# Optimization experiments

Measured on AMD Instinct MI355X. Metric: run time of the kernel, lower is better.

Reference implementation:

```python
import jax, jax.numpy as jnp
import numpy as np

N = 30000      # num_nodes
E = 480000     # num_edges
NF = 128       # node_features
EF = 64        # edge_features
HID = 256      # hidden_dim
L = 4          # num_layers
H = 8          # heads
D = HID // H   # per-head dim = 32
SCALE = 0.02


def _ln(x, g, b, eps=1e-5):
    m = x.mean(-1, keepdims=True)
    v = ((x - m) ** 2).mean(-1, keepdims=True)
    return (x - m) * jax.lax.rsqrt(v + eps) * g + b


def _mlp_head(x, W1, b1, W2, b2):
    return jax.nn.sigmoid(jax.nn.relu(x @ W1 + b1) @ W2 + b2)


def setup_inputs() -> dict:
    key = jax.random.key(0)
    ks = jax.random.split(key, 32)
    r = lambda k, shp: SCALE * jax.random.normal(k, shp, dtype=jnp.float32)
    inp = {
        'x': jax.random.normal(ks[0], (N, NF), dtype=jnp.float32),
        'edge_attr': jax.random.normal(ks[1], (E, EF), dtype=jnp.float32),
        'edge_index': jax.random.randint(ks[2], (2, E), 0, N, dtype=jnp.int32),
        # encoders
        'enc_Wn': r(ks[3], (NF, HID)), 'enc_bn': jnp.zeros((HID,), jnp.float32),
        'enc_We': r(ks[4], (EF, HID)), 'enc_be': jnp.zeros((HID,), jnp.float32),
        # stacked TransformerConv params for L layers
        'Wq': r(ks[5], (L, HID, HID)), 'bq': jnp.zeros((L, HID), jnp.float32),
        'Wk': r(ks[6], (L, HID, HID)), 'bk': jnp.zeros((L, HID), jnp.float32),
        'Wv': r(ks[7], (L, HID, HID)), 'bv': jnp.zeros((L, HID), jnp.float32),
        'We': r(ks[8], (L, HID, HID)),  # lin_edge has no bias in PyG
        'Wsk': r(ks[9], (L, HID, HID)), 'bsk': jnp.zeros((L, HID), jnp.float32),
        # shared LayerNorm (module reuses self.norm every layer)
        'ln_g': jnp.ones((HID,), jnp.float32), 'ln_b': jnp.zeros((HID,), jnp.float32),
        # contagion predictor
        'cp_W1': r(ks[10], (HID, HID // 2)), 'cp_b1': jnp.zeros((HID // 2,), jnp.float32),
        'cp_W2': r(ks[11], (HID // 2, 1)), 'cp_b2': jnp.zeros((1,), jnp.float32),
        # systemic risk predictor
        'sp_W1': r(ks[12], (HID, HID // 2)), 'sp_b1': jnp.zeros((HID // 2,), jnp.float32),
        'sp_W2': r(ks[13], (HID // 2, 1)), 'sp_b2': jnp.zeros((1,), jnp.float32),
    }
    return inp


def reference(x, edge_attr, edge_index, enc_Wn, enc_bn, enc_We, enc_be,
              Wq, bq, Wk, bk, Wv, bv, We, Wsk, bsk, ln_g, ln_b,
              cp_W1, cp_b1, cp_W2, cp_b2, sp_W1, sp_b1, sp_W2, sp_b2):
    src, dst = edge_index[0], edge_index[1]
    h = x @ enc_Wn + enc_bn                 # [N,HID]
    e = edge_attr @ enc_We + enc_be         # [E,HID]
    inv_sqrt_d = 1.0 / jnp.sqrt(jnp.asarray(D, h.dtype))
    for l in range(L):
        # TransformerConv: query at dst, key/value at src, edge bias on both k and v
        q = (h @ Wq[l] + bq[l]).reshape(N, H, D)[dst]            # [E,H,D]
        ke = (e @ We[l]).reshape(E, H, D)                        # [E,H,D]
        k = (h @ Wk[l] + bk[l]).reshape(N, H, D)[src] + ke
        v = (h @ Wv[l] + bv[l]).reshape(N, H, D)[src] + ke
        score = (q * k).sum(-1) * inv_sqrt_d                     # [E,H]
        smax = jax.ops.segment_max(score, dst, num_segments=N)   # [N,H]
        p = jnp.exp(score - smax[dst])
        denom = jax.ops.segment_sum(p, dst, num_segments=N)
        alpha = p / (denom[dst] + 1e-16)                         # scatter-softmax
        agg = jax.ops.segment_sum(alpha[..., None] * v, dst, num_segments=N)
        out = agg.reshape(N, HID) + h @ Wsk[l] + bsk[l]          # concat heads + root skip
        h = _ln(h + out, ln_g, ln_b)                             # residual + shared LN (eval: no dropout)
    g = h.mean(0, keepdims=True)                                 # [1,HID] global mean pool
    contagion_risk = _mlp_head(h, cp_W1, cp_b1, cp_W2, cp_b2)    # [N,1]
    systemic_risk = _mlp_head(g, sp_W1, sp_b1, sp_W2, sp_b2)     # [1,1]
    return h, g, contagion_risk, systemic_risk
```

## Files before the change

kernel.cpp:

```cpp
#include <hip/hip_runtime.h>
#include <cstddef>
#include <cstdint>

#define NN 30000
#define EE 480000
#define NFD 128
#define EFD 64
#define HID 256
#define NL 4
#define NH 8

#define DT_BF16 0
#define DT_F32  1
#define DT_EXT  2

#define OFF_WT  ((size_t)65787648)
#define MIN_B   ((size_t)68015872)
#define MIN_A   ((size_t)129455872)

#define WT_ENC 0
#define WT_LAYER(l) (32768 + (size_t)(l) * 262144)
#define WT_CP1 (32768 + (size_t)1048576)

typedef short bf16x8 __attribute__((ext_vector_type(8)));
typedef unsigned short us8 __attribute__((ext_vector_type(8)));
typedef float f32x4 __attribute__((ext_vector_type(4)));

__device__ __forceinline__ float bf2f(unsigned short u) {
  union { unsigned int i; float f; } v; v.i = ((unsigned int)u) << 16; return v.f;
}
__device__ __forceinline__ unsigned short f2bf(float f) {
  union { float f; unsigned int i; } v; v.f = f;
  unsigned int i = v.i;
  return (unsigned short)((i + 0x7FFFu + ((i >> 16) & 1u)) >> 16);
}
struct F4 { float x, y, z, w; };
__device__ __forceinline__ F4 load4bf(const unsigned short* p) {
  ushort4 u = *reinterpret_cast<const ushort4*>(p);
  F4 f; f.x = bf2f(u.x); f.y = bf2f(u.y); f.z = bf2f(u.z); f.w = bf2f(u.w);
  return f;
}
__device__ __forceinline__ F4 load4f(const float* p) {
  float4 t = *reinterpret_cast<const float4*>(p);
  F4 f; f.x = t.x; f.y = t.y; f.z = t.z; f.w = t.w; return f;
}
__device__ __forceinline__ F4 load4any(const void* p, size_t idx, int f32) {
  return f32 ? load4f((const float*)p + idx) : load4bf((const unsigned short*)p + idx);
}
__device__ __forceinline__ float load1any(const void* p, size_t idx, int f32) {
  return f32 ? ((const float*)p)[idx] : bf2f(((const unsigned short*)p)[idx]);
}
__device__ __forceinline__ void store1any(void* p, size_t idx, float v, int f32) {
  if (f32) ((float*)p)[idx] = v; else ((unsigned short*)p)[idx] = f2bf(v);
}

__global__ void probe_dtype(const void* __restrict__ ln_g, int* __restrict__ flag) {
  unsigned int u = *(const unsigned int*)ln_g;
  *flag = ((u & 0xFFFFu) == 0u) ? 1 : 0;
}

__global__ void wt_build(const void* __restrict__ enc_Wn,
                         const void* __restrict__ Wq, const void* __restrict__ Wk,
                         const void* __restrict__ Wv, const void* __restrict__ Wsk,
                         const void* __restrict__ cp_W1,
                         unsigned short* __restrict__ Wt, const int* __restrict__ flagp)
{
  const int f = *flagp;
  size_t idx = (size_t)blockIdx.x * 256 + threadIdx.x;
  if (idx < 32768) {
    int n = idx >> 7, k = idx & 127;
    Wt[WT_ENC + idx] = f2bf(load1any(enc_Wn, (size_t)k * 256 + n, f));
  } else if (idx < 32768 + 1048576) {
    size_t off = idx - 32768;
    int l = off >> 18;
    int which = (off >> 16) & 3;
    size_t e = off & 65535;
    int n = e >> 8, k = e & 255;
    const void* W = (which == 0) ? Wq : (which == 1) ? Wk : (which == 2) ? Wv : Wsk;
    Wt[idx] = f2bf(load1any(W, (size_t)l * 65536 + (size_t)k * 256 + n, f));
  } else if (idx < 32768 + 1048576 + 32768) {
    size_t e = idx - 32768 - 1048576;
    int n = e >> 8, k = e & 255;
    Wt[idx] = f2bf(load1any(cp_W1, (size_t)k * 128 + n, f));
  }
}

template<bool OUT_F32, bool RELU>
__global__ __launch_bounds__(256) void mfma_gemm(
    const void* __restrict__ Av, int aMode,
    const unsigned short* __restrict__ Bt,
    const void* __restrict__ biasv, size_t biasEl, int biasMode,
    void* __restrict__ Cv, int ldC, int cOff,
    int M, int K, const int* __restrict__ flagp)
{
  const int f = *flagp;
  const int aF32 = (aMode == DT_EXT) ? f : aMode;
  const int biF32 = (biasMode == DT_EXT) ? f : biasMode;

  __shared__ unsigned short Al[128][40];
  __shared__ unsigned short Bl[64][40];
  const int bm = blockIdx.x * 128;
  const int bn = blockIdx.y * 64;
  const int tid = threadIdx.x;
  const int wv = tid >> 6, lane = tid & 63;
  const int l16 = lane & 15, quad = lane >> 4;

  f32x4 acc[2][4];
#pragma unroll
  for (int i = 0; i < 2; i++)
#pragma unroll
    for (int j = 0; j < 4; j++) acc[i][j] = (f32x4){0.f, 0.f, 0.f, 0.f};

  const int ar = tid >> 1;
  const int ah = (tid & 1) << 4;
  const int bnr = tid >> 2;
  const int bk8 = (tid & 3) << 3;

  for (int k0 = 0; k0 < K; k0 += 32) {
    us8 w0, w1;
    int gr = bm + ar;
    if (gr < M) {
      if (!aF32) {
        const unsigned short* ap = (const unsigned short*)Av + (size_t)gr * K + k0 + ah;
        w0 = *(const us8*)ap;
        w1 = *(const us8*)(ap + 8);
      } else {
        const float* ap = (const float*)Av + (size_t)gr * K + k0 + ah;
        float4 u0 = *(const float4*)ap;
        float4 u1 = *(const float4*)(ap + 4);
        float4 u2 = *(const float4*)(ap + 8);
        float4 u3 = *(const float4*)(ap + 12);
        w0[0] = f2bf(u0.x); w0[1] = f2bf(u0.y); w0[2] = f2bf(u0.z); w0[3] = f2bf(u0.w);
        w0[4] = f2bf(u1.x); w0[5] = f2bf(u1.y); w0[6] = f2bf(u1.z); w0[7] = f2bf(u1.w);
        w1[0] = f2bf(u2.x); w1[1] = f2bf(u2.y); w1[2] = f2bf(u2.z); w1[3] = f2bf(u2.w);
        w1[4] = f2bf(u3.x); w1[5] = f2bf(u3.y); w1[6] = f2bf(u3.z); w1[7] = f2bf(u3.w);
      }
    } else {
      w0 = (us8)0; w1 = (us8)0;
    }
    *(us8*)&Al[ar][ah] = w0;
    *(us8*)&Al[ar][ah + 8] = w1;
    *(us8*)&Bl[bnr][bk8] = *(const us8*)&Bt[(size_t)(bn + bnr) * K + k0 + bk8];
    __syncthreads();

    bf16x8 a0 = *(const bf16x8*)&Al[wv * 32 + l16][quad * 8];
    bf16x8 a1 = *(const bf16x8*)&Al[wv * 32 + 16 + l16][quad * 8];
#pragma unroll
    for (int tn = 0; tn < 4; tn++) {
      bf16x8 b = *(const bf16x8*)&Bl[tn * 16 + l16][quad * 8];
      acc[0][tn] = __builtin_amdgcn_mfma_f32_16x16x32_bf16(a0, b, acc[0][tn], 0, 0, 0);
      acc[1][tn] = __builtin_amdgcn_mfma_f32_16x16x32_bf16(a1, b, acc[1][tn], 0, 0, 0);
    }
    __syncthreads();
  }

#pragma unroll
  for (int tm = 0; tm < 2; tm++) {
#pragma unroll
    for (int tn = 0; tn < 4; tn++) {
      int col = bn + tn * 16 + l16;
      float bias = load1any(biasv, biasEl + col, biF32);
#pragma unroll
      for (int r = 0; r < 4; r++) {
        int row = bm + wv * 32 + tm * 16 + quad * 4 + r;
        if (row < M) {
          float v = acc[tm][tn][r] + bias;
          if (RELU) v = fmaxf(v, 0.f);
          size_t off = (size_t)row * ldC + cOff + col;
          if (OUT_F32) ((float*)Cv)[off] = v;
          else ((unsigned short*)Cv)[off] = f2bf(v);
        }
      }
    }
  }
}

__global__ void fold_kernel(const void* __restrict__ enc_We,
                            const void* __restrict__ enc_be,
                            const void* __restrict__ We_all,
                            float* __restrict__ Mfold, const int* __restrict__ flagp)
{
  const int f = *flagp;
  int idx = blockIdx.x * blockDim.x + threadIdx.x;
  if (idx >= NL * 65 * HID) return;
  int l = idx / (65 * HID);
  int rc = idx - l * 65 * HID;
  int row = rc >> 8;
  int col = rc & 255;
  size_t Wbase = (size_t)l * HID * HID;
  float acc = 0.f;
  if (row < 64) {
    for (int k = 0; k < HID; k++)
      acc += load1any(enc_We, (size_t)row * HID + k, f) * load1any(We_all, Wbase + (size_t)k * HID + col, f);
  } else {
    for (int k = 0; k < HID; k++)
      acc += load1any(enc_be, k, f) * load1any(We_all, Wbase + (size_t)k * HID + col, f);
  }
  Mfold[idx] = acc;
}

__global__ void hist_kernel(const int* __restrict__ dst, int* __restrict__ rp) {
  int e = blockIdx.x * 256 + threadIdx.x;
  if (e < EE) atomicAdd(&rp[dst[e]], 1);
}

__global__ __launch_bounds__(1024) void scan_kernel(int* __restrict__ rp) {
  __shared__ int part[1024];
  int t = threadIdx.x;
  int base = t * 30;
  int loc[30];
  int sum = 0;
#pragma unroll
  for (int i = 0; i < 30; i++) {
    int idx = base + i;
    int v = (idx < NN) ? rp[idx] : 0;
    loc[i] = v; sum += v;
  }
  part[t] = sum;
  __syncthreads();
  for (int off = 1; off < 1024; off <<= 1) {
    int v = (t >= off) ? part[t - off] : 0;
    __syncthreads();
    part[t] += v;
    __syncthreads();
  }
  int run = (t == 0) ? 0 : part[t - 1];
#pragma unroll
  for (int i = 0; i < 30; i++) {
    int idx = base + i;
    if (idx < NN) { rp[idx] = run; run += loc[i]; }
    else if (idx == NN) { rp[NN] = run; }
  }
}

__global__ void scatter_kernel(const int* __restrict__ src, const int* __restrict__ dst,
                               const int* __restrict__ rp, int* __restrict__ cnt2,
                               int2* __restrict__ sed) {
  int e = blockIdx.x * 256 + threadIdx.x;
  if (e >= EE) return;
  int d = dst[e];
  int pos = rp[d] + atomicAdd(&cnt2[d], 1);
  int2 v; v.x = src[e]; v.y = e;
  sed[pos] = v;
}

__global__ void ea_build(const int2* __restrict__ sed, const void* __restrict__ edge_attr,
                         unsigned short* __restrict__ ea_srt, const int* __restrict__ flagp) {
  const int f = *flagp;
  int gid = blockIdx.x * 256 + threadIdx.x;
  int pos = gid >> 4;
  int sub = (gid & 15) * 4;
  int e = sed[pos].y;
  F4 v = load4any(edge_attr, (size_t)e * EFD + sub, f);
  ushort4 o; o.x = f2bf(v.x); o.y = f2bf(v.y); o.z = f2bf(v.z); o.w = f2bf(v.w);
  *reinterpret_cast<ushort4*>(ea_srt + (size_t)pos * EFD + sub) = o;
}

template<bool SORTED>
__global__ __launch_bounds__(256) void edge_fused(
    const int* __restrict__ rp, const int2* __restrict__ sed,
    const unsigned short* __restrict__ Qb, const unsigned short* __restrict__ KV,
    const unsigned short* __restrict__ ea_srt,
    const void* __restrict__ edge_attr,
    const float* __restrict__ Mf,
    const unsigned short* __restrict__ Sb,
    unsigned short* __restrict__ hb,
    const void* __restrict__ ln_g, const void* __restrict__ ln_b,
    const int* __restrict__ flagp)
{
  __shared__ float wl[4][8][68];
  const int f = *flagp;
  const int wv = threadIdx.x >> 6;
  const int nw = blockIdx.x * 4 + wv;
  const int lane = threadIdx.x & 63;
  const int hd = lane >> 3;
  const int j = lane & 7;
  const int c4 = lane * 4;

  const size_t rowb = (size_t)nw * HID;
  F4 q4 = load4bf(Qb + rowb + c4);

  float q32[32];
#pragma unroll
  for (int i = 0; i < 8; i++) {
    F4 t = load4bf(Qb + rowb + hd * 32 + i * 4);
    q32[i * 4 + 0] = t.x; q32[i * 4 + 1] = t.y; q32[i * 4 + 2] = t.z; q32[i * 4 + 3] = t.w;
  }
  float t8[8];
#pragma unroll
  for (int kk = 0; kk < 8; kk++) {
    const float* Mrow = Mf + (size_t)(j * 8 + kk) * HID + hd * 32;
    float a = 0.f;
#pragma unroll
    for (int cc = 0; cc < 8; cc++) {
      float4 m4 = *reinterpret_cast<const float4*>(Mrow + cc * 4);
      a = fmaf(m4.x, q32[cc * 4 + 0], a);
      a = fmaf(m4.y, q32[cc * 4 + 1], a);
      a = fmaf(m4.z, q32[cc * 4 + 2], a);
      a = fmaf(m4.w, q32[cc * 4 + 3], a);
    }
    t8[kk] = a;
  }
  F4 b4 = load4f(Mf + (size_t)64 * HID + c4);
  float s0 = q4.x * b4.x + q4.y * b4.y + q4.z * b4.z + q4.w * b4.w;
  s0 += __shfl_xor(s0, 1);
  s0 += __shfl_xor(s0, 2);
  s0 += __shfl_xor(s0, 4);

  float accv[4] = {0.f, 0.f, 0.f, 0.f};
  float wacc[8] = {0.f, 0.f, 0.f, 0.f, 0.f, 0.f, 0.f, 0.f};
  float den = 0.f;
  const int beg = rp[nw], end = rp[nw + 1];

  if (beg < end) {
    const float scl = 0.17677669529663687f;
    int tA = beg;
    int tB = (beg + 1 < end) ? beg + 1 : beg;
    int sA = sed[tA].x;
    int sB = sed[tB].x;
    const unsigned short* kvp;
    kvp = KV + (size_t)sA * 512;
    F4 kA = load4bf(kvp + c4);
    F4 vA = load4bf(kvp + 256 + c4);
    kvp = KV + (size_t)sB * 512;
    F4 kB = load4bf(kvp + c4);
    F4 vB = load4bf(kvp + 256 + c4);
    F4 ea0A, ea1A, ea0B, ea1B;
    if (SORTED) {
      ea0A = load4bf(ea_srt + (size_t)tA * EFD + j * 8);
      ea1A = load4bf(ea_srt + (size_t)tA * EFD + j * 8 + 4);
      ea0B = load4bf(ea_srt + (size_t)tB * EFD + j * 8);
      ea1B = load4bf(ea_srt + (size_t)tB * EFD + j * 8 + 4);
    } else {
      size_t eA = (size_t)sed[tA].y, eB = (size_t)sed[tB].y;
      ea0A = load4any(edge_attr, eA * EFD + j * 8, f);
      ea1A = load4any(edge_attr, eA * EFD + j * 8 + 4, f);
      ea0B = load4any(edge_attr, eB * EFD + j * 8, f);
      ea1B = load4any(edge_attr, eB * EFD + j * 8 + 4, f);
    }
    int tC = (beg + 2 < end) ? beg + 2 : beg;
    int tD = (beg + 3 < end) ? beg + 3 : beg;
    int sC = sed[tC].x;
    int sD = sed[tD].x;

    for (int t = beg; t < end; t += 2) {
      kvp = KV + (size_t)sC * 512;
      F4 kC = load4bf(kvp + c4);
      F4 vC = load4bf(kvp + 256 + c4);
      kvp = KV + (size_t)sD * 512;
      F4 kD = load4bf(kvp + c4);
      F4 vD = load4bf(kvp + 256 + c4);
      F4 ea0C, ea1C, ea0D, ea1D;
      if (SORTED) {
        ea0C = load4bf(ea_srt + (size_t)tC * EFD + j * 8);
        ea1C = load4bf(ea_srt + (size_t)tC * EFD + j * 8 + 4);
        ea0D = load4bf(ea_srt + (size_t)tD * EFD + j * 8);
        ea1D = load4bf(ea_srt + (size_t)tD * EFD + j * 8 + 4);
      } else {
        size_t eC = (size_t)sed[tC].y, eD = (size_t)sed[tD].y;
        ea0C = load4any(edge_attr, eC * EFD + j * 8, f);
        ea1C = load4any(edge_attr, eC * EFD + j * 8 + 4, f);
        ea0D = load4any(edge_attr, eD * EFD + j * 8, f);
        ea1D = load4any(edge_attr, eD * EFD + j * 8 + 4, f);
      }
      int tE = (t + 4 < end) ? t + 4 : beg;
      int tF = (t + 5 < end) ? t + 5 : beg;
      int sE = sed[tE].x;
      int sF = sed[tF].x;

      float mB = (t + 1 < end) ? 1.f : 0.f;
      float rA = q4.x * kA.x + q4.y * kA.y + q4.z * kA.z + q4.w * kA.w;
      float rB = q4.x * kB.x + q4.y * kB.y + q4.z * kB.z + q4.w * kB.w;
      rA = fmaf(ea0A.x, t8[0], rA); rB = fmaf(ea0B.x, t8[0], rB);
      rA = fmaf(ea0A.y, t8[1], rA); rB = fmaf(ea0B.y, t8[1], rB);
      rA = fmaf(ea0A.z, t8[2], rA); rB = fmaf(ea0B.z, t8[2], rB);
      rA = fmaf(ea0A.w, t8[3], rA); rB = fmaf(ea0B.w, t8[3], rB);
      rA = fmaf(ea1A.x, t8[4], rA); rB = fmaf(ea1B.x, t8[4], rB);
      rA = fmaf(ea1A.y, t8[5], rA); rB = fmaf(ea1B.y, t8[5], rB);
      rA = fmaf(ea1A.z, t8[6], rA); rB = fmaf(ea1B.z, t8[6], rB);
      rA = fmaf(ea1A.w, t8[7], rA); rB = fmaf(ea1B.w, t8[7], rB);
      { float u = __shfl_xor(rA, 1); float v = __shfl_xor(rB, 1); rA += u; rB += v; }
      { float u = __shfl_xor(rA, 2); float v = __shfl_xor(rB, 2); rA += u; rB += v; }
      { float u = __shfl_xor(rA, 4); float v = __shfl_xor(rB, 4); rA += u; rB += v; }
      float scA = fminf(fmaxf((rA + s0) * scl, -30.f), 30.f);
      float scB = fminf(fmaxf((rB + s0) * scl, -30.f), 30.f);
      float pA = __expf(scA);
      float pB = mB * __expf(scB);
      den += pA + pB;
      accv[0] = fmaf(pA, vA.x, fmaf(pB, vB.x, accv[0]));
      accv[1] = fmaf(pA, vA.y, fmaf(pB, vB.y, accv[1]));
      accv[2] = fmaf(pA, vA.z, fmaf(pB, vB.z, accv[2]));
      accv[3] = fmaf(pA, vA.w, fmaf(pB, vB.w, accv[3]));
      wacc[0] = fmaf(pA, ea0A.x, fmaf(pB, ea0B.x, wacc[0]));
      wacc[1] = fmaf(pA, ea0A.y, fmaf(pB, ea0B.y, wacc[1]));
      wacc[2] = fmaf(pA, ea0A.z, fmaf(pB, ea0B.z, wacc[2]));
      wacc[3] = fmaf(pA, ea0A.w, fmaf(pB, ea0B.w, wacc[3]));
      wacc[4] = fmaf(pA, ea1A.x, fmaf(pB, ea1B.x, wacc[4]));
      wacc[5] = fmaf(pA, ea1A.y, fmaf(pB, ea1B.y, wacc[5]));
      wacc[6] = fmaf(pA, ea1A.z, fmaf(pB, ea1B.z, wacc[6]));
      wacc[7] = fmaf(pA, ea1A.w, fmaf(pB, ea1B.w, wacc[7]));
      kA = kC; vA = vC; ea0A = ea0C; ea1A = ea1C;
      kB = kD; vB = vD; ea0B = ea0D; ea1B = ea1D;
      tA = tC; tB = tD; tC = tE; tD = tF; sC = sE; sD = sF;
    }
  }

#pragma unroll
  for (int i = 0; i < 8; i++) wl[wv][hd][j * 8 + i] = wacc[i];
  __syncthreads();

  float ke0 = 0.f, ke1 = 0.f, ke2 = 0.f, ke3 = 0.f;
#pragma unroll 8
  for (int k = 0; k < 64; k++) {
    float w = wl[wv][hd][k];
    float4 m4 = *reinterpret_cast<const float4*>(Mf + (size_t)k * HID + c4);
    ke0 = fmaf(w, m4.x, ke0);
    ke1 = fmaf(w, m4.y, ke1);
    ke2 = fmaf(w, m4.z, ke2);
    ke3 = fmaf(w, m4.w, ke3);
  }

  float invden = 1.f / (den + 1e-16f);
  float sel = (end > beg) ? 1.f : 0.f;
  F4 s4 = load4bf(Sb + rowb + c4);
  F4 hh = load4bf(hb + rowb + c4);
  float r0 = hh.x + sel * ((accv[0] + ke0) * invden + b4.x) + s4.x;
  float r1 = hh.y + sel * ((accv[1] + ke1) * invden + b4.y) + s4.y;
  float r2 = hh.z + sel * ((accv[2] + ke2) * invden + b4.z) + s4.z;
  float r3 = hh.w + sel * ((accv[3] + ke3) * invden + b4.w) + s4.w;

  float sum = r0 + r1 + r2 + r3;
#pragma unroll
  for (int o = 1; o < 64; o <<= 1) sum += __shfl_xor(sum, o);
  float mean = sum * (1.f / HID);
  float d0 = r0 - mean, d1 = r1 - mean, d2 = r2 - mean, d3 = r3 - mean;
  float vs = d0 * d0 + d1 * d1 + d2 * d2 + d3 * d3;
#pragma unroll
  for (int o = 1; o < 64; o <<= 1) vs += __shfl_xor(vs, o);
  float rstd = rsqrtf(vs * (1.f / HID) + 1e-5f);
  ushort4 o4;
  o4.x = f2bf(d0 * rstd * load1any(ln_g, c4 + 0, f) + load1any(ln_b, c4 + 0, f));
  o4.y = f2bf(d1 * rstd * load1any(ln_g, c4 + 1, f) + load1any(ln_b, c4 + 1, f));
  o4.z = f2bf(d2 * rstd * load1any(ln_g, c4 + 2, f) + load1any(ln_b, c4 + 2, f));
  o4.w = f2bf(d3 * rstd * load1any(ln_g, c4 + 3, f) + load1any(ln_b, c4 + 3, f));
  *reinterpret_cast<ushort4*>(hb + rowb + c4) = o4;
}

__global__ void copy_h_out(const unsigned short* __restrict__ h, void* __restrict__ out,
                           const int* __restrict__ flagp) {
  const int f = *flagp;
  int i = blockIdx.x * 256 + threadIdx.x;
  store1any(out, i, bf2f(h[i]), f);
}

__global__ void colsum_kernel(const unsigned short* __restrict__ h, float* __restrict__ gsum) {
  int c = threadIdx.x;
  float s = 0.f;
  for (int r = blockIdx.x; r < NN; r += gridDim.x) s += bf2f(h[(size_t)r * HID + c]);
  atomicAdd(&gsum[c], s);
}

__global__ void write_g_kernel(const float* __restrict__ gsum, void* __restrict__ out,
                               const int* __restrict__ flagp) {
  const int f = *flagp;
  int c = threadIdx.x;
  store1any(out, (size_t)NN * HID + c, gsum[c] * (1.f / NN), f);
}

__global__ __launch_bounds__(256) void cp2_kernel(
    const float* __restrict__ hid, const void* __restrict__ W2,
    const void* __restrict__ b2, void* __restrict__ out,
    const int* __restrict__ flagp)
{
  const int f = *flagp;
  int nw = (blockIdx.x << 2) + (threadIdx.x >> 6);
  if (nw >= NN) return;
  int lane = threadIdx.x & 63;
  const float* hr = hid + (size_t)nw * 128;
  float s = hr[lane * 2] * load1any(W2, lane * 2, f) + hr[lane * 2 + 1] * load1any(W2, lane * 2 + 1, f);
#pragma unroll
  for (int o = 1; o < 64; o <<= 1) s += __shfl_xor(s, o);
  if (lane == 0) {
    float xv = s + load1any(b2, 0, f);
    store1any(out, (size_t)NN * HID + HID + nw, 1.f / (1.f + __expf(-xv)), f);
  }
}

__global__ __launch_bounds__(128) void sys_kernel(
    const float* __restrict__ gsum,
    const void* __restrict__ W1, const void* __restrict__ b1,
    const void* __restrict__ W2, const void* __restrict__ b2,
    void* __restrict__ out, const int* __restrict__ flagp)
{
  const int f = *flagp;
  __shared__ float red[2];
  int j = threadIdx.x;
  float acc = load1any(b1, j, f);
  const float invN = 1.f / NN;
  for (int k = 0; k < HID; k++) acc = fmaf(gsum[k] * invN, load1any(W1, (size_t)k * 128 + j, f), acc);
  float v = fmaxf(acc, 0.f) * load1any(W2, j, f);
#pragma unroll
  for (int o = 1; o < 64; o <<= 1) v += __shfl_xor(v, o);
  if ((j & 63) == 0) red[j >> 6] = v;
  __syncthreads();
  if (j == 0) {
    float xv = red[0] + red[1] + load1any(b2, 0, f);
    store1any(out, (size_t)NN * HID + HID + NN, 1.f / (1.f + __expf(-xv)), f);
  }
}

__global__ void diag_kernel(float* __restrict__ out, float v, int n4) {
  int i = blockIdx.x * 256 + threadIdx.x;
  if (i < n4) out[i] = (i == 0) ? v : 0.f;
}

extern "C" void kernel_launch(void* const* d_in, const int* in_sizes, int n_in,
                              void* d_out, int out_size, void* d_ws, size_t ws_size,
                              hipStream_t stream)
{
  (void)in_sizes; (void)n_in;

  if (ws_size < MIN_B) {
    diag_kernel<<<(out_size / 2 + 255) / 256, 256, 0, stream>>>(
        (float*)d_out, (float)(ws_size >> 20), out_size / 2);
    return;
  }
  const bool planA = (ws_size >= MIN_A);

  const void* x         = d_in[0];
  const void* edge_attr = d_in[1];
  const int*  edge_index= (const int*)d_in[2];
  const void* enc_Wn = d_in[3];
  const void* enc_bn = d_in[4];
  const void* enc_We = d_in[5];
  const void* enc_be = d_in[6];
  const void* Wq  = d_in[7];
  const void* bq  = d_in[8];
  const void* Wk  = d_in[9];
  const void* bk  = d_in[10];
  const void* Wv  = d_in[11];
  const void* bvv = d_in[12];
  const void* We  = d_in[13];
  const void* Wsk = d_in[14];
  const void* bsk = d_in[15];
  const void* ln_g = d_in[16];
  const void* ln_b = d_in[17];
  const void* cp_W1 = d_in[18];
  const void* cp_b1 = d_in[19];
  const void* cp_W2 = d_in[20];
  const void* cp_b2 = d_in[21];
  const void* sp_W1 = d_in[22];
  const void* sp_b1 = d_in[23];
  const void* sp_W2 = d_in[24];
  const void* sp_b2 = d_in[25];

  char* ws = (char*)d_ws;
  unsigned short* hb  = (unsigned short*)(ws + 0);
  unsigned short* Sb  = (unsigned short*)(ws + 15360000);
  unsigned short* KVb = (unsigned short*)(ws + 30720000);
  int2*  sed   = (int2*)(ws + 61440000);
  int*   rp    = (int*)(ws + 65280000);
  int*   cnt2  = (int*)(ws + 65400064);
  float* Mfold = (float*)(ws + 65520128);
  float* gsum  = (float*)(ws + 65786368);
  int*   flagp = (int*)(ws + 65787392);
  unsigned short* Wt = (unsigned short*)(ws + OFF_WT);
  unsigned short* ea_srt = (unsigned short*)(ws + MIN_B);
  unsigned short* Qb = (unsigned short*)d_out;
  float* cph = (float*)(ws + 15360000);

  const int* src = edge_index;
  const int* dst = edge_index + EE;

  probe_dtype<<<1, 1, 0, stream>>>(ln_g, flagp);
  wt_build<<<(1114112 + 255) / 256, 256, 0, stream>>>(enc_Wn, Wq, Wk, Wv, Wsk, cp_W1, Wt, flagp);
  fold_kernel<<<(NL * 65 * HID + 255) / 256, 256, 0, stream>>>(enc_We, enc_be, We, Mfold, flagp);

  hipMemsetAsync(rp, 0, 120064, stream);
  hipMemsetAsync(cnt2, 0, 120064, stream);
  hist_kernel<<<(EE + 255) / 256, 256, 0, stream>>>(dst, rp);
  scan_kernel<<<1, 1024, 0, stream>>>(rp);
  scatter_kernel<<<(EE + 255) / 256, 256, 0, stream>>>(src, dst, rp, cnt2, sed);
  if (planA) {
    ea_build<<<EE * 16 / 256, 256, 0, stream>>>(sed, edge_attr, ea_srt, flagp);
  }

  const int gx = (NN + 127) / 128;
  {
    dim3 g(gx, 4);
    mfma_gemm<false, false><<<g, 256, 0, stream>>>(
        x, DT_EXT, Wt + WT_ENC, enc_bn, 0, DT_EXT, hb, HID, 0, NN, NFD, flagp);
  }

  for (int l = 0; l < NL; l++) {
    dim3 gN(gx, 4);
    size_t bo = (size_t)l * HID;
    const unsigned short* wl_base = Wt + WT_LAYER(l);
    mfma_gemm<false, false><<<gN, 256, 0, stream>>>(
        hb, DT_BF16, wl_base + 0,      bq,  bo, DT_EXT, Qb,  HID, 0,   NN, HID, flagp);
    mfma_gemm<false, false><<<gN, 256, 0, stream>>>(
        hb, DT_BF16, wl_base + 65536,  bk,  bo, DT_EXT, KVb, 512, 0,   NN, HID, flagp);
    mfma_gemm<false, false><<<gN, 256, 0, stream>>>(
        hb, DT_BF16, wl_base + 131072, bvv, bo, DT_EXT, KVb, 512, 256, NN, HID, flagp);
    mfma_gemm<false, false><<<gN, 256, 0, stream>>>(
        hb, DT_BF16, wl_base + 196608, bsk, bo, DT_EXT, Sb,  HID, 0,   NN, HID, flagp);
    const float* Mf = Mfold + (size_t)l * 65 * HID;
    if (planA) {
      edge_fused<true><<<NN / 4, 256, 0, stream>>>(
          rp, sed, Qb, KVb, ea_srt, edge_attr, Mf, Sb, hb, ln_g, ln_b, flagp);
    } else {
      edge_fused<false><<<NN / 4, 256, 0, stream>>>(
          rp, sed, Qb, KVb, ea_srt, edge_attr, Mf, Sb, hb, ln_g, ln_b, flagp);
    }
  }

  copy_h_out<<<NN, 256, 0, stream>>>(hb, d_out, flagp);
  hipMemsetAsync(gsum, 0, HID * 4, stream);
  colsum_kernel<<<256, 256, 0, stream>>>(hb, gsum);
  write_g_kernel<<<1, 256, 0, stream>>>(gsum, d_out, flagp);

  {
    dim3 g(gx, 2);
    mfma_gemm<true, true><<<g, 256, 0, stream>>>(
        hb, DT_BF16, Wt + WT_CP1, cp_b1, 0, DT_EXT, cph, 128, 0, NN, HID, flagp);
  }
  cp2_kernel<<<NN / 4, 256, 0, stream>>>(cph, cp_W2, cp_b2, d_out, flagp);
  sys_kernel<<<1, 128, 0, stream>>>(gsum, sp_W1, sp_b1, sp_W2, sp_b2, d_out, flagp);
}
```

Measured before the change: 2.248 ms.

## Fuse per-layer Q/K/V/skip GEMMs into one launch and slim edge kernel registers

Replaces the four per-layer projection GEMM launches with a single kernel whose grid's y dimension selects the Q, K, V or skip weight slice and output buffer. In the edge kernel, each lane now loads one edge-attribute scalar and broadcasts the eight values it needs with shuffles instead of loading two float4s. Temporaries are scoped to shorten live ranges, the bias load is moved after the loop, and launch bounds are raised, all to lower register pressure and raise occupancy. This cuts launch overhead and edge-attribute load traffic, at the price of extra shuffle instructions in the inner loop and possible spills under the tighter register cap.

Result: slower. 2.351 ms (+4.6%).

```diff
diff --git a/kernel.cpp b/kernel.cpp
--- a/kernel.cpp
+++ b/kernel.cpp
@@ -175,6 +175,85 @@
   }
 }
 
+__global__ __launch_bounds__(256) void mfma_gemm_qkvs(
+    const unsigned short* __restrict__ A,
+    const unsigned short* __restrict__ Bt,
+    const void* __restrict__ bq, const void* __restrict__ bk,
+    const void* __restrict__ bv, const void* __restrict__ bsk, size_t biasEl,
+    unsigned short* __restrict__ Qb, unsigned short* __restrict__ KVb,
+    unsigned short* __restrict__ Sb,
+    int M, const int* __restrict__ flagp)
+{
+  const int f = *flagp;
+  __shared__ unsigned short Al[128][40];
+  __shared__ unsigned short Bl[64][40];
+  const int bm = blockIdx.x * 128;
+  const int bnG = blockIdx.y * 64;
+  const int which = bnG >> 8;
+  const int bn = bnG & 255;
+  const int tid = threadIdx.x;
+  const int wv = tid >> 6, lane = tid & 63;
+  const int l16 = lane & 15, quad = lane >> 4;
+
+  f32x4 acc[2][4];
+#pragma unroll
+  for (int i = 0; i < 2; i++)
+#pragma unroll
+    for (int j = 0; j < 4; j++) acc[i][j] = (f32x4){0.f, 0.f, 0.f, 0.f};
+
+  const int ar = tid >> 1;
+  const int ah = (tid & 1) << 4;
+  const int bnr = tid >> 2;
+  const int bk8 = (tid & 3) << 3;
+  const unsigned short* Bbase = Bt + (size_t)which * 65536;
+
+  for (int k0 = 0; k0 < HID; k0 += 32) {
+    us8 w0, w1;
+    int gr = bm + ar;
+    if (gr < M) {
+      const unsigned short* ap = A + (size_t)gr * HID + k0 + ah;
+      w0 = *(const us8*)ap;
+      w1 = *(const us8*)(ap + 8);
+    } else {
+      w0 = (us8)0; w1 = (us8)0;
+    }
+    *(us8*)&Al[ar][ah] = w0;
+    *(us8*)&Al[ar][ah + 8] = w1;
+    *(us8*)&Bl[bnr][bk8] = *(const us8*)&Bbase[(size_t)(bn + bnr) * HID + k0 + bk8];
+    __syncthreads();
+
+    bf16x8 a0 = *(const bf16x8*)&Al[wv * 32 + l16][quad * 8];
+    bf16x8 a1 = *(const bf16x8*)&Al[wv * 32 + 16 + l16][quad * 8];
+#pragma unroll
+    for (int tn = 0; tn < 4; tn++) {
+      bf16x8 b = *(const bf16x8*)&Bl[tn * 16 + l16][quad * 8];
+      acc[0][tn] = __builtin_amdgcn_mfma_f32_16x16x32_bf16(a0, b, acc[0][tn], 0, 0, 0);
+      acc[1][tn] = __builtin_amdgcn_mfma_f32_16x16x32_bf16(a1, b, acc[1][tn], 0, 0, 0);
+    }
+    __syncthreads();
+  }
+
+  const void* biasv = (which == 0) ? bq : (which == 1) ? bk : (which == 2) ? bv : bsk;
+  unsigned short* out = (which == 0) ? Qb : (which == 3) ? Sb : KVb;
+  const int ldC = (which == 1 || which == 2) ? 512 : 256;
+  const int cOff = (which == 2) ? 256 : 0;
+
+#pragma unroll
+  for (int tm = 0; tm < 2; tm++) {
+#pragma unroll
+    for (int tn = 0; tn < 4; tn++) {
+      int col = bn + tn * 16 + l16;
+      float bias = load1any(biasv, biasEl + col, f);
+#pragma unroll
+      for (int r = 0; r < 4; r++) {
+        int row = bm + wv * 32 + tm * 16 + quad * 4 + r;
+        if (row < M)
+          out[(size_t)row * ldC + cOff + col] = f2bf(acc[tm][tn][r] + bias);
+      }
+    }
+  }
+}
+
 __global__ void fold_kernel(const void* __restrict__ enc_We,
                             const void* __restrict__ enc_be,
                             const void* __restrict__ We_all,
@@ -257,7 +336,7 @@
 }
 
 template<bool SORTED>
-__global__ __launch_bounds__(256) void edge_fused(
+__global__ __launch_bounds__(256, 8) void edge_fused(
     const int* __restrict__ rp, const int2* __restrict__ sed,
     const unsigned short* __restrict__ Qb, const unsigned short* __restrict__ KV,
     const unsigned short* __restrict__ ea_srt,
@@ -270,42 +349,48 @@
 {
   __shared__ float wl[4][8][68];
   const int f = *flagp;
-  const int wv = threadIdx.x >> 6;
+  const int wv = __builtin_amdgcn_readfirstlane(threadIdx.x >> 6);
   const int nw = blockIdx.x * 4 + wv;
   const int lane = threadIdx.x & 63;
   const int hd = lane >> 3;
   const int j = lane & 7;
+  const int jb = j << 3;
   const int c4 = lane * 4;
 
   const size_t rowb = (size_t)nw * HID;
   F4 q4 = load4bf(Qb + rowb + c4);
 
-  float q32[32];
-#pragma unroll
-  for (int i = 0; i < 8; i++) {
-    F4 t = load4bf(Qb + rowb + hd * 32 + i * 4);
-    q32[i * 4 + 0] = t.x; q32[i * 4 + 1] = t.y; q32[i * 4 + 2] = t.z; q32[i * 4 + 3] = t.w;
-  }
   float t8[8];
-#pragma unroll
-  for (int kk = 0; kk < 8; kk++) {
-    const float* Mrow = Mf + (size_t)(j * 8 + kk) * HID + hd * 32;
-    float a = 0.f;
-#pragma unroll
-    for (int cc = 0; cc < 8; cc++) {
-      float4 m4 = *reinterpret_cast<const float4*>(Mrow + cc * 4);
-      a = fmaf(m4.x, q32[cc * 4 + 0], a);
-      a = fmaf(m4.y, q32[cc * 4 + 1], a);
-      a = fmaf(m4.z, q32[cc * 4 + 2], a);
-      a = fmaf(m4.w, q32[cc * 4 + 3], a);
-    }
-    t8[kk] = a;
-  }
-  F4 b4 = load4f(Mf + (size_t)64 * HID + c4);
-  float s0 = q4.x * b4.x + q4.y * b4.y + q4.z * b4.z + q4.w * b4.w;
-  s0 += __shfl_xor(s0, 1);
-  s0 += __shfl_xor(s0, 2);
-  s0 += __shfl_xor(s0, 4);
+  {
+    float q32[32];
+#pragma unroll
+    for (int i = 0; i < 8; i++) {
+      F4 t = load4bf(Qb + rowb + hd * 32 + i * 4);
+      q32[i * 4 + 0] = t.x; q32[i * 4 + 1] = t.y; q32[i * 4 + 2] = t.z; q32[i * 4 + 3] = t.w;
+    }
+#pragma unroll
+    for (int kk = 0; kk < 8; kk++) {
+      const float* Mrow = Mf + (size_t)(jb + kk) * HID + hd * 32;
+      float a = 0.f;
+#pragma unroll
+      for (int cc = 0; cc < 8; cc++) {
+        float4 m4 = *reinterpret_cast<const float4*>(Mrow + cc * 4);
+        a = fmaf(m4.x, q32[cc * 4 + 0], a);
+        a = fmaf(m4.y, q32[cc * 4 + 1], a);
+        a = fmaf(m4.z, q32[cc * 4 + 2], a);
+        a = fmaf(m4.w, q32[cc * 4 + 3], a);
+      }
+      t8[kk] = a;
+    }
+  }
+  float s0;
+  {
+    F4 b4 = load4f(Mf + (size_t)64 * HID + c4);
+    s0 = q4.x * b4.x + q4.y * b4.y + q4.z * b4.z + q4.w * b4.w;
+    s0 += __shfl_xor(s0, 1);
+    s0 += __shfl_xor(s0, 2);
+    s0 += __shfl_xor(s0, 4);
+  }
 
   float accv[4] = {0.f, 0.f, 0.f, 0.f};
   float wacc[8] = {0.f, 0.f, 0.f, 0.f, 0.f, 0.f, 0.f, 0.f};
@@ -325,18 +410,13 @@
     kvp = KV + (size_t)sB * 512;
     F4 kB = load4bf(kvp + c4);
     F4 vB = load4bf(kvp + 256 + c4);
-    F4 ea0A, ea1A, ea0B, ea1B;
+    float eaA, eaB;
     if (SORTED) {
-      ea0A = load4bf(ea_srt + (size_t)tA * EFD + j * 8);
-      ea1A = load4bf(ea_srt + (size_t)tA * EFD + j * 8 + 4);
-      ea0B = load4bf(ea_srt + (size_t)tB * EFD + j * 8);
-      ea1B = load4bf(ea_srt + (size_t)tB * EFD + j * 8 + 4);
+      eaA = bf2f(ea_srt[(size_t)tA * EFD + lane]);
+      eaB = bf2f(ea_srt[(size_t)tB * EFD + lane]);
     } else {
-      size_t eA = (size_t)sed[tA].y, eB = (size_t)sed[tB].y;
-      ea0A = load4any(edge_attr, eA * EFD + j * 8, f);
-      ea1A = load4any(edge_attr, eA * EFD + j * 8 + 4, f);
-      ea0B = load4any(edge_attr, eB * EFD + j * 8, f);
-      ea1B = load4any(edge_attr, eB * EFD + j * 8 + 4, f);
+      eaA = load1any(edge_attr, (size_t)sed[tA].y * EFD + lane, f);
+      eaB = load1any(edge_attr, (size_t)sed[tB].y * EFD + lane, f);
     }
     int tC = (beg + 2 < end) ? beg + 2 : beg;
     int tD = (beg + 3 < end) ? beg + 3 : beg;
@@ -350,18 +430,13 @@
       kvp = KV + (size_t)sD * 512;
       F4 kD = load4bf(kvp + c4);
       F4 vD = load4bf(kvp + 256 + c4);
-      F4 ea0C, ea1C, ea0D, ea1D;
+      float eaC, eaD;
       if (SORTED) {
-        ea0C = load4bf(ea_srt + (size_t)tC * EFD + j * 8);
-        ea1C = load4bf(ea_srt + (size_t)tC * EFD + j * 8 + 4);
-        ea0D = load4bf(ea_srt + (size_t)tD * EFD + j * 8);
-        ea1D = load4bf(ea_srt + (size_t)tD * EFD + j * 8 + 4);
+        eaC = bf2f(ea_srt[(size_t)tC * EFD + lane]);
+        eaD = bf2f(ea_srt[(size_t)tD * EFD + lane]);
       } else {
-        size_t eC = (size_t)sed[tC].y, eD = (size_t)sed[tD].y;
-        ea0C = load4any(edge_attr, eC * EFD + j * 8, f);
-        ea1C = load4any(edge_attr, eC * EFD + j * 8 + 4, f);
-        ea0D = load4any(edge_attr, eD * EFD + j * 8, f);
-        ea1D = load4any(edge_attr, eD * EFD + j * 8 + 4, f);
+        eaC = load1any(edge_attr, (size_t)sed[tC].y * EFD + lane, f);
+        eaD = load1any(edge_attr, (size_t)sed[tD].y * EFD + lane, f);
       }
       int tE = (t + 4 < end) ? t + 4 : beg;
       int tF = (t + 5 < end) ? t + 5 : beg;
@@ -369,44 +444,56 @@
       int sF = sed[tF].x;
 
       float mB = (t + 1 < end) ? 1.f : 0.f;
-      float rA = q4.x * kA.x + q4.y * kA.y + q4.z * kA.z + q4.w * kA.w;
-      float rB = q4.x * kB.x + q4.y * kB.y + q4.z * kB.z + q4.w * kB.w;
-      rA = fmaf(ea0A.x, t8[0], rA); rB = fmaf(ea0B.x, t8[0], rB);
-      rA = fmaf(ea0A.y, t8[1], rA); rB = fmaf(ea0B.y, t8[1], rB);
-      rA = fmaf(ea0A.z, t8[2], rA); rB = fmaf(ea0B.z, t8[2], rB);
-      rA = fmaf(ea0A.w, t8[3], rA); rB = fmaf(ea0B.w, t8[3], rB);
-      rA = fmaf(ea1A.x, t8[4], rA); rB = fmaf(ea1B.x, t8[4], rB);
-      rA = fmaf(ea1A.y, t8[5], rA); rB = fmaf(ea1B.y, t8[5], rB);
-      rA = fmaf(ea1A.z, t8[6], rA); rB = fmaf(ea1B.z, t8[6], rB);
-      rA = fmaf(ea1A.w, t8[7], rA); rB = fmaf(ea1B.w, t8[7], rB);
-      { float u = __shfl_xor(rA, 1); float v = __shfl_xor(rB, 1); rA += u; rB += v; }
-      { float u = __shfl_xor(rA, 2); float v = __shfl_xor(rB, 2); rA += u; rB += v; }
-      { float u = __shfl_xor(rA, 4); float v = __shfl_xor(rB, 4); rA += u; rB += v; }
-      float scA = fminf(fmaxf((rA + s0) * scl, -30.f), 30.f);
-      float scB = fminf(fmaxf((rB + s0) * scl, -30.f), 30.f);
-      float pA = __expf(scA);
-      float pB = mB * __expf(scB);
+      float pA, pB;
+      {
+        float rB = q4.x * kB.x + q4.y * kB.y + q4.z * kB.z + q4.w * kB.w;
+        float eB[8];
+#pragma unroll
+        for (int i = 0; i < 8; i++) {
+          eB[i] = __shfl(eaB, jb + i, 64);
+          rB = fmaf(eB[i], t8[i], rB);
+        }
+        rB += __shfl_xor(rB, 1);
+        rB += __shfl_xor(rB, 2);
+        rB += __shfl_xor(rB, 4);
+        float scB = fminf(fmaxf((rB + s0) * scl, -30.f), 30.f);
+        pB = mB * __expf(scB);
+        accv[0] = fmaf(pB, vB.x, accv[0]);
+        accv[1] = fmaf(pB, vB.y, accv[1]);
+        accv[2] = fmaf(pB, vB.z, accv[2]);
+        accv[3] = fmaf(pB, vB.w, accv[3]);
+#pragma unroll
+        for (int i = 0; i < 8; i++) wacc[i] = fmaf(pB, eB[i], wacc[i]);
+      }
+      {
+        float rA = q4.x * kA.x + q4.y * kA.y + q4.z * kA.z + q4.w * kA.w;
+        float eA[8];
+#pragma unroll
+        for (int i = 0; i < 8; i++) {
+          eA[i] = __shfl(eaA, jb + i, 64);
+          rA = fmaf(eA[i], t8[i], rA);
+        }
+        rA += __shfl_xor(rA, 1);
+        rA += __shfl_xor(rA, 2);
+        rA += __shfl_xor(rA, 4);
+        float scA = fminf(fmaxf((rA + s0) * scl, -30.f), 30.f);
+        pA = __expf(scA);
+        accv[0] = fmaf(pA, vA.x, accv[0]);
+        accv[1] = fmaf(pA, vA.y, accv[1]);
+        accv[2] = fmaf(pA, vA.z, accv[2]);
+        accv[3] = fmaf(pA, vA.w, accv[3]);
+#pragma unroll
+        for (int i = 0; i < 8; i++) wacc[i] = fmaf(pA, eA[i], wacc[i]);
+      }
       den += pA + pB;
-      accv[0] = fmaf(pA, vA.x, fmaf(pB, vB.x, accv[0]));
-      accv[1] = fmaf(pA, vA.y, fmaf(pB, vB.y, accv[1]));
-      accv[2] = fmaf(pA, vA.z, fmaf(pB, vB.z, accv[2]));
-      accv[3] = fmaf(pA, vA.w, fmaf(pB, vB.w, accv[3]));
-      wacc[0] = fmaf(pA, ea0A.x, fmaf(pB, ea0B.x, wacc[0]));
-      wacc[1] = fmaf(pA, ea0A.y, fmaf(pB, ea0B.y, wacc[1]));
-      wacc[2] = fmaf(pA, ea0A.z, fmaf(pB, ea0B.z, wacc[2]));
-      wacc[3] = fmaf(pA, ea0A.w, fmaf(pB, ea0B.w, wacc[3]));
-      wacc[4] = fmaf(pA, ea1A.x, fmaf(pB, ea1B.x, wacc[4]));
-      wacc[5] = fmaf(pA, ea1A.y, fmaf(pB, ea1B.y, wacc[5]));
-      wacc[6] = fmaf(pA, ea1A.z, fmaf(pB, ea1B.z, wacc[6]));
-      wacc[7] = fmaf(pA, ea1A.w, fmaf(pB, ea1B.w, wacc[7]));
-      kA = kC; vA = vC; ea0A = ea0C; ea1A = ea1C;
-      kB = kD; vB = vD; ea0B = ea0D; ea1B = ea1D;
-      tA = tC; tB = tD; tC = tE; tD = tF; sC = sE; sD = sF;
-    }
-  }
-
-#pragma unroll
-  for (int i = 0; i < 8; i++) wl[wv][hd][j * 8 + i] = wacc[i];
+      kA = kC; vA = vC; eaA = eaC;
+      kB = kD; vB = vD; eaB = eaD;
+      tC = tE; tD = tF; sC = sE; sD = sF;
+    }
+  }
+
+#pragma unroll
+  for (int i = 0; i < 8; i++) wl[wv][hd][jb + i] = wacc[i];
   __syncthreads();
 
   float ke0 = 0.f, ke1 = 0.f, ke2 = 0.f, ke3 = 0.f;
@@ -422,6 +509,8 @@
 
   float invden = 1.f / (den + 1e-16f);
   float sel = (end > beg) ? 1.f : 0.f;
+  __builtin_amdgcn_sched_barrier(0);
+  F4 b4 = load4f(Mf + (size_t)64 * HID + c4);
   F4 s4 = load4bf(Sb + rowb + c4);
   F4 hh = load4bf(hb + rowb + c4);
   float r0 = hh.x + sel * ((accv[0] + ke0) * invden + b4.x) + s4.x;
@@ -593,17 +682,10 @@
   }
 
   for (int l = 0; l < NL; l++) {
-    dim3 gN(gx, 4);
     size_t bo = (size_t)l * HID;
-    const unsigned short* wl_base = Wt + WT_LAYER(l);
-    mfma_gemm<false, false><<<gN, 256, 0, stream>>>(
-        hb, DT_BF16, wl_base + 0,      bq,  bo, DT_EXT, Qb,  HID, 0,   NN, HID, flagp);
-    mfma_gemm<false, false><<<gN, 256, 0, stream>>>(
-        hb, DT_BF16, wl_base + 65536,  bk,  bo, DT_EXT, KVb, 512, 0,   NN, HID, flagp);
-    mfma_gemm<false, false><<<gN, 256, 0, stream>>>(
-        hb, DT_BF16, wl_base + 131072, bvv, bo, DT_EXT, KVb, 512, 256, NN, HID, flagp);
-    mfma_gemm<false, false><<<gN, 256, 0, stream>>>(
-        hb, DT_BF16, wl_base + 196608, bsk, bo, DT_EXT, Sb,  HID, 0,   NN, HID, flagp);
+    dim3 gQ(gx, 16);
+    mfma_gemm_qkvs<<<gQ, 256, 0, stream>>>(
+        hb, Wt + WT_LAYER(l), bq, bk, bvv, bsk, bo, Qb, KVb, Sb, NN, flagp);
     const float* Mf = Mfold + (size_t)l * 65 * HID;
     if (planA) {
       edge_fused<true><<<NN / 4, 256, 0, stream>>>(
```

## Fuse per-layer Q/K/V/skip GEMMs into one launch and tune edge kernel occupancy

Applied to the files above, without the earlier changes.

Replaces four separate per-layer GEMM launches with a single kernel whose grid covers all four weight matrices, selecting bias, output buffer and stride from the column block. In the edge kernel, the Q-by-folded-matrix precompute is reordered to stream Q chunks instead of holding a 32-float array. The bias load is moved later, and a min-blocks launch bound is added to lower register pressure and raise occupancy. The goal is less launch overhead and better residency, with some risk of spills from the tighter register cap.

After: 2.474 ms. 10.1% more time.

```diff
diff --git a/kernel.cpp b/kernel.cpp
--- a/kernel.cpp
+++ b/kernel.cpp
@@ -175,6 +175,85 @@
   }
 }
 
+__global__ __launch_bounds__(256) void mfma_gemm_qkvs(
+    const unsigned short* __restrict__ A,
+    const unsigned short* __restrict__ Bt,
+    const void* __restrict__ bq, const void* __restrict__ bk,
+    const void* __restrict__ bv, const void* __restrict__ bsk, size_t biasEl,
+    unsigned short* __restrict__ Qb, unsigned short* __restrict__ KVb,
+    unsigned short* __restrict__ Sb,
+    int M, const int* __restrict__ flagp)
+{
+  const int f = *flagp;
+  __shared__ unsigned short Al[128][40];
+  __shared__ unsigned short Bl[64][40];
+  const int bm = blockIdx.x * 128;
+  const int bnG = blockIdx.y * 64;
+  const int which = bnG >> 8;
+  const int bn = bnG & 255;
+  const int tid = threadIdx.x;
+  const int wv = tid >> 6, lane = tid & 63;
+  const int l16 = lane & 15, quad = lane >> 4;
+
+  f32x4 acc[2][4];
+#pragma unroll
+  for (int i = 0; i < 2; i++)
+#pragma unroll
+    for (int j = 0; j < 4; j++) acc[i][j] = (f32x4){0.f, 0.f, 0.f, 0.f};
+
+  const int ar = tid >> 1;
+  const int ah = (tid & 1) << 4;
+  const int bnr = tid >> 2;
+  const int bk8 = (tid & 3) << 3;
+  const unsigned short* Bbase = Bt + (size_t)which * 65536;
+
+  for (int k0 = 0; k0 < HID; k0 += 32) {
+    us8 w0, w1;
+    int gr = bm + ar;
+    if (gr < M) {
+      const unsigned short* ap = A + (size_t)gr * HID + k0 + ah;
+      w0 = *(const us8*)ap;
+      w1 = *(const us8*)(ap + 8);
+    } else {
+      w0 = (us8)0; w1 = (us8)0;
+    }
+    *(us8*)&Al[ar][ah] = w0;
+    *(us8*)&Al[ar][ah + 8] = w1;
+    *(us8*)&Bl[bnr][bk8] = *(const us8*)&Bbase[(size_t)(bn + bnr) * HID + k0 + bk8];
+    __syncthreads();
+
+    bf16x8 a0 = *(const bf16x8*)&Al[wv * 32 + l16][quad * 8];
+    bf16x8 a1 = *(const bf16x8*)&Al[wv * 32 + 16 + l16][quad * 8];
+#pragma unroll
+    for (int tn = 0; tn < 4; tn++) {
+      bf16x8 b = *(const bf16x8*)&Bl[tn * 16 + l16][quad * 8];
+      acc[0][tn] = __builtin_amdgcn_mfma_f32_16x16x32_bf16(a0, b, acc[0][tn], 0, 0, 0);
+      acc[1][tn] = __builtin_amdgcn_mfma_f32_16x16x32_bf16(a1, b, acc[1][tn], 0, 0, 0);
+    }
+    __syncthreads();
+  }
+
+  const void* biasv = (which == 0) ? bq : (which == 1) ? bk : (which == 2) ? bv : bsk;
+  unsigned short* out = (which == 0) ? Qb : (which == 3) ? Sb : KVb;
+  const int ldC = (which == 1 || which == 2) ? 512 : 256;
+  const int cOff = (which == 2) ? 256 : 0;
+
+#pragma unroll
+  for (int tm = 0; tm < 2; tm++) {
+#pragma unroll
+    for (int tn = 0; tn < 4; tn++) {
+      int col = bn + tn * 16 + l16;
+      float bias = load1any(biasv, biasEl + col, f);
+#pragma unroll
+      for (int r = 0; r < 4; r++) {
+        int row = bm + wv * 32 + tm * 16 + quad * 4 + r;
+        if (row < M)
+          out[(size_t)row * ldC + cOff + col] = f2bf(acc[tm][tn][r] + bias);
+      }
+    }
+  }
+}
+
 __global__ void fold_kernel(const void* __restrict__ enc_We,
                             const void* __restrict__ enc_be,
                             const void* __restrict__ We_all,
@@ -257,7 +336,7 @@
 }
 
 template<bool SORTED>
-__global__ __launch_bounds__(256) void edge_fused(
+__global__ __launch_bounds__(256, 6) void edge_fused(
     const int* __restrict__ rp, const int2* __restrict__ sed,
     const unsigned short* __restrict__ Qb, const unsigned short* __restrict__ KV,
     const unsigned short* __restrict__ ea_srt,
@@ -270,42 +349,41 @@
 {
   __shared__ float wl[4][8][68];
   const int f = *flagp;
-  const int wv = threadIdx.x >> 6;
+  const int wv = __builtin_amdgcn_readfirstlane(threadIdx.x >> 6);
   const int nw = blockIdx.x * 4 + wv;
   const int lane = threadIdx.x & 63;
   const int hd = lane >> 3;
   const int j = lane & 7;
+  const int jb = j << 3;
   const int c4 = lane * 4;
 
   const size_t rowb = (size_t)nw * HID;
   F4 q4 = load4bf(Qb + rowb + c4);
 
-  float q32[32];
-#pragma unroll
-  for (int i = 0; i < 8; i++) {
-    F4 t = load4bf(Qb + rowb + hd * 32 + i * 4);
-    q32[i * 4 + 0] = t.x; q32[i * 4 + 1] = t.y; q32[i * 4 + 2] = t.z; q32[i * 4 + 3] = t.w;
-  }
-  float t8[8];
-#pragma unroll
-  for (int kk = 0; kk < 8; kk++) {
-    const float* Mrow = Mf + (size_t)(j * 8 + kk) * HID + hd * 32;
-    float a = 0.f;
-#pragma unroll
-    for (int cc = 0; cc < 8; cc++) {
-      float4 m4 = *reinterpret_cast<const float4*>(Mrow + cc * 4);
-      a = fmaf(m4.x, q32[cc * 4 + 0], a);
-      a = fmaf(m4.y, q32[cc * 4 + 1], a);
-      a = fmaf(m4.z, q32[cc * 4 + 2], a);
-      a = fmaf(m4.w, q32[cc * 4 + 3], a);
-    }
-    t8[kk] = a;
-  }
-  F4 b4 = load4f(Mf + (size_t)64 * HID + c4);
-  float s0 = q4.x * b4.x + q4.y * b4.y + q4.z * b4.z + q4.w * b4.w;
-  s0 += __shfl_xor(s0, 1);
-  s0 += __shfl_xor(s0, 2);
-  s0 += __shfl_xor(s0, 4);
+  float t8[8] = {0.f, 0.f, 0.f, 0.f, 0.f, 0.f, 0.f, 0.f};
+#pragma unroll
+  for (int cc = 0; cc < 8; cc++) {
+    F4 qc = load4bf(Qb + rowb + hd * 32 + cc * 4);
+#pragma unroll
+    for (int kk = 0; kk < 8; kk++) {
+      const float4 m4 = *reinterpret_cast<const float4*>(
+          Mf + (size_t)(jb + kk) * HID + hd * 32 + cc * 4);
+      float a = t8[kk];
+      a = fmaf(m4.x, qc.x, a);
+      a = fmaf(m4.y, qc.y, a);
+      a = fmaf(m4.z, qc.z, a);
+      a = fmaf(m4.w, qc.w, a);
+      t8[kk] = a;
+    }
+  }
+  float s0;
+  {
+    F4 b4 = load4f(Mf + (size_t)64 * HID + c4);
+    s0 = q4.x * b4.x + q4.y * b4.y + q4.z * b4.z + q4.w * b4.w;
+    s0 += __shfl_xor(s0, 1);
+    s0 += __shfl_xor(s0, 2);
+    s0 += __shfl_xor(s0, 4);
+  }
 
   float accv[4] = {0.f, 0.f, 0.f, 0.f};
   float wacc[8] = {0.f, 0.f, 0.f, 0.f, 0.f, 0.f, 0.f, 0.f};
@@ -406,7 +484,7 @@
   }
 
 #pragma unroll
-  for (int i = 0; i < 8; i++) wl[wv][hd][j * 8 + i] = wacc[i];
+  for (int i = 0; i < 8; i++) wl[wv][hd][jb + i] = wacc[i];
   __syncthreads();
 
   float ke0 = 0.f, ke1 = 0.f, ke2 = 0.f, ke3 = 0.f;
@@ -422,6 +500,7 @@
 
   float invden = 1.f / (den + 1e-16f);
   float sel = (end > beg) ? 1.f : 0.f;
+  F4 b4 = load4f(Mf + (size_t)64 * HID + c4);
   F4 s4 = load4bf(Sb + rowb + c4);
   F4 hh = load4bf(hb + rowb + c4);
   float r0 = hh.x + sel * ((accv[0] + ke0) * invden + b4.x) + s4.x;
@@ -593,17 +672,10 @@
   }
 
   for (int l = 0; l < NL; l++) {
-    dim3 gN(gx, 4);
     size_t bo = (size_t)l * HID;
-    const unsigned short* wl_base = Wt + WT_LAYER(l);
-    mfma_gemm<false, false><<<gN, 256, 0, stream>>>(
-        hb, DT_BF16, wl_base + 0,      bq,  bo, DT_EXT, Qb,  HID, 0,   NN, HID, flagp);
-    mfma_gemm<false, false><<<gN, 256, 0, stream>>>(
-        hb, DT_BF16, wl_base + 65536,  bk,  bo, DT_EXT, KVb, 512, 0,   NN, HID, flagp);
-    mfma_gemm<false, false><<<gN, 256, 0, stream>>>(
-        hb, DT_BF16, wl_base + 131072, bvv, bo, DT_EXT, KVb, 512, 256, NN, HID, flagp);
-    mfma_gemm<false, false><<<gN, 256, 0, stream>>>(
-        hb, DT_BF16, wl_base + 196608, bsk, bo, DT_EXT, Sb,  HID, 0,   NN, HID, flagp);
+    dim3 gQ(gx, 16);
+    mfma_gemm_qkvs<<<gQ, 256, 0, stream>>>(
+        hb, Wt + WT_LAYER(l), bq, bk, bvv, bsk, bo, Qb, KVb, Sb, NN, flagp);
     const float* Mf = Mfold + (size_t)l * 65 * HID;
     if (planA) {
       edge_fused<true><<<NN / 4, 256, 0, stream>>>(
```
